# Optimization experiments

Hardware: AMD Instinct MI355X
Metric: run time of the kernel (lower is better)

Reference implementation:

```python
import jax, jax.numpy as jnp
import numpy as np

B, N, D = 4, 4096, 256
EPS = 1e-5


def setup_inputs() -> dict:
    key = jax.random.key(0)
    ks = jax.random.split(key, 6)
    x = jax.random.normal(ks[0], (B, N, D), dtype=jnp.float32)
    coord = jax.random.normal(ks[1], (B, N, D), dtype=jnp.float32)
    ln_g = jnp.ones((D,), dtype=jnp.float32)
    ln_b = jnp.zeros((D,), dtype=jnp.float32)
    s = 1.0 / np.sqrt(D)
    w_qkv = jax.random.normal(ks[2], (D, 3 * D), dtype=jnp.float32) * s
    w_out = jax.random.normal(ks[3], (D, D), dtype=jnp.float32) * s
    b_out = jnp.zeros((D,), dtype=jnp.float32)
    return {"x": x, "coord": coord, "ln_g": ln_g, "ln_b": ln_b,
            "w_qkv": w_qkv, "w_out": w_out, "b_out": b_out}


def reference(x, coord, ln_g, ln_b, w_qkv, w_out, b_out):
    d = x.shape[-1]
    scale = d ** (-0.5)
    # LayerNorm over last dim
    mu = jnp.mean(x, axis=-1, keepdims=True)
    var = jnp.var(x, axis=-1, keepdims=True)
    nx = (x - mu) * jax.lax.rsqrt(var + EPS) * ln_g + ln_b
    # QKV projection (no bias), chunk into q,k,v
    qkv = jnp.einsum('bnd,de->bne', nx, w_qkv)
    q, k, v = jnp.split(qkv, 3, axis=-1)
    # coord bias on q and k (module does NOT split into heads)
    q = q + coord
    k = k + coord
    dots = jnp.einsum('bnd,bmd->bnm', q, k) * scale
    attn = jax.nn.softmax(dots, axis=-1)
    out = jnp.einsum('bnm,bmd->bnd', attn, v)
    return jnp.einsum('bnd,de->bne', out, w_out) + b_out
```

## Files before the change

### kernel.cpp

```cpp
#include <hip/hip_runtime.h>
#include <hip/hip_fp16.h>
#include <math.h>

constexpr int B = 4, N = 4096, D = 256;
constexpr int BN = B * N;
constexpr float EPS = 1e-5f;
constexpr float QSC2 = 0.0625f * 1.44269504088896340736f;

constexpr int SPLIT = 4;
constexpr int KVB = 32;
constexpr int NTK = (N / SPLIT) / KVB;
constexpr float THR = 8.0f;

typedef __attribute__((ext_vector_type(8))) _Float16 f16x8;
typedef __attribute__((ext_vector_type(2))) __fp16 fp16x2;
typedef __attribute__((ext_vector_type(4))) float f32x4;
typedef __attribute__((ext_vector_type(16))) float f32x16;

__device__ inline f32x4 mfma_f16(f16x8 a, f16x8 b, f32x4 c) {
  return __builtin_amdgcn_mfma_f32_16x16x32_f16(a, b, c, 0, 0, 0);
}
__device__ inline f32x16 mfma32(f16x8 a, f16x8 b, f32x16 c) {
  return __builtin_amdgcn_mfma_f32_32x32x16_f16(a, b, c, 0, 0, 0);
}
__device__ inline ushort f2h(float x) {
  __half h = __float2half(x);
  return *(ushort*)&h;
}
__device__ inline float h2f(ushort u) {
  __half h;
  *(ushort*)&h = u;
  return __half2float(h);
}
__device__ inline unsigned pkh(float a, float b) {
  fp16x2 r = __builtin_amdgcn_cvt_pkrtz(a, b);
  return *(unsigned*)&r;
}
__device__ inline void gload16(const ushort* g, ushort* l) {
  __builtin_amdgcn_global_load_lds(
      (const __attribute__((address_space(1))) void*)g,
      (__attribute__((address_space(3))) void*)l, 16, 0, 0);
}

__global__ __launch_bounds__(256) void ln_kernel(
    const float* __restrict__ x, const float* __restrict__ g,
    const float* __restrict__ bta, ushort* __restrict__ nxh,
    ushort* __restrict__ nxl) {
  const int row = blockIdx.x;
  const int t = threadIdx.x;
  const float v = x[(size_t)row * D + t];
  float s = v, ss = v * v;
#pragma unroll
  for (int o = 32; o > 0; o >>= 1) {
    s += __shfl_down(s, o);
    ss += __shfl_down(ss, o);
  }
  __shared__ float red[8];
  if ((t & 63) == 0) {
    red[t >> 6] = s;
    red[(t >> 6) + 4] = ss;
  }
  __syncthreads();
  s = red[0] + red[1] + red[2] + red[3];
  ss = red[4] + red[5] + red[6] + red[7];
  const float mu = s * (1.0f / D);
  const float var = ss * (1.0f / D) - mu * mu;
  const float rsig = rsqrtf(var + EPS);
  const float nx = (v - mu) * rsig * g[t] + bta[t];
  const ushort h = f2h(nx);
  nxh[(size_t)row * D + t] = h;
  nxl[(size_t)row * D + t] = f2h(nx - h2f(h));
}

__global__ __launch_bounds__(256) void castw_kernel(
    const float* __restrict__ w_qkv, const float* __restrict__ w_out,
    ushort* __restrict__ wt, ushort* __restrict__ wot) {
  const int id = blockIdx.x * 256 + threadIdx.x;
  if (id < 768 * 256) {
    const int n = id >> 8, k = id & 255;
    wt[id] = f2h(w_qkv[(size_t)k * 768 + n]);
  } else {
    const int j = id - 768 * 256;
    const int n = j >> 8, k = j & 255;
    wot[j] = f2h(w_out[(size_t)k * 256 + n]);
  }
}

__global__ __launch_bounds__(256, 4) void qkv_kernel(
    const ushort* __restrict__ nxh, const ushort* __restrict__ nxl,
    const ushort* __restrict__ wt, const float* __restrict__ coord,
    ushort* __restrict__ qfp, ushort* __restrict__ kfp,
    ushort* __restrict__ vtp) {
  const int t = threadIdx.x;
  const int w = t >> 6, lane = t & 63;
  const int lrow = lane & 15, lhi = lane >> 4;
  const int m0 = blockIdx.x * 128 + w * 32;
  const int c0 = blockIdx.y * 64;
  f32x4 acc[2][4];
#pragma unroll
  for (int qs = 0; qs < 2; ++qs)
#pragma unroll
    for (int nt = 0; nt < 4; ++nt) acc[qs][nt] = f32x4{0.f, 0.f, 0.f, 0.f};

#pragma unroll
  for (int kc = 0; kc < D; kc += 32) {
    f16x8 ah[2], al[2], bw[4];
#pragma unroll
    for (int qs = 0; qs < 2; ++qs) {
      const size_t ao = (size_t)(m0 + qs * 16 + lrow) * D + kc + lhi * 8;
      ah[qs] = *(const f16x8*)(nxh + ao);
      al[qs] = *(const f16x8*)(nxl + ao);
    }
#pragma unroll
    for (int nt = 0; nt < 4; ++nt)
      bw[nt] = *(const f16x8*)(wt + (size_t)(c0 + nt * 16 + lrow) * D + kc +
                               lhi * 8);
#pragma unroll
    for (int qs = 0; qs < 2; ++qs)
#pragma unroll
      for (int nt = 0; nt < 4; ++nt) {
        acc[qs][nt] = mfma_f16(ah[qs], bw[nt], acc[qs][nt]);
        acc[qs][nt] = mfma_f16(al[qs], bw[nt], acc[qs][nt]);
      }
  }

  const int region = blockIdx.y >> 2;
  const int cbase = c0 & 255;
  if (region < 2) {
    const float sc = (region == 0) ? QSC2 : 1.0f;
    ushort* dp = (region == 0) ? qfp : kfp;
#pragma unroll
    for (int qs = 0; qs < 2; ++qs)
#pragma unroll
      for (int nt = 0; nt < 4; ++nt)
#pragma unroll
        for (int i = 0; i < 4; ++i) {
          const int row = m0 + qs * 16 + lhi * 4 + i;
          const int col = cbase + nt * 16 + lrow;
          const float val =
              (acc[qs][nt][i] + coord[(size_t)row * D + col]) * sc;
          dp[(size_t)row * D + col] = f2h(val);
        }
  } else {
#pragma unroll
    for (int qs = 0; qs < 2; ++qs)
#pragma unroll
      for (int nt = 0; nt < 4; ++nt)
#pragma unroll
        for (int i = 0; i < 4; ++i) {
          const int row = m0 + qs * 16 + lhi * 4 + i;
          const int col = cbase + nt * 16 + lrow;
          const int bb = row >> 12, n = row & (N - 1);
          vtp[((size_t)bb * D + col) * N + n] = f2h(acc[qs][nt][i]);
        }
  }
}

__global__ __launch_bounds__(512, 2) void attn_kernel(
    const ushort* __restrict__ qf, const ushort* __restrict__ kf,
    const ushort* __restrict__ vt, ushort* __restrict__ pob,
    float* __restrict__ mlb) {
  __shared__ ushort kbuf[3][8192];
  __shared__ ushort vbuf[3][8192];

  const int tid = threadIdx.x;
  const int lane = tid & 63;
  const int q = lane & 31, h = lane >> 5;
  const int w = tid >> 6;
  const int b = blockIdx.y, s = blockIdx.z;
  const int qw = blockIdx.x * 256 + w * 32;
  const int kbeg = s * (N / SPLIT);

  const ushort* qrow = qf + ((size_t)b * N + qw + q) * D;
  const ushort* kfb = kf + (size_t)b * N * D;
  const ushort* vtb = vt + (size_t)b * D * N;
  ushort* pog = pob + (size_t)s * BN * D;
  float* mlg = mlb + (size_t)s * BN * 2;

  f16x8 qfr[8];
#pragma unroll
  for (int c = 0; c < 8; ++c)
    qfr[c] = *(const f16x8*)(qrow + c * 16 + h * 8);

  f32x16 o[8];
#pragma unroll
  for (int dt = 0; dt < 8; ++dt)
#pragma unroll
    for (int r = 0; r < 16; ++r) o[dt][r] = 0.f;
  float m = -1e30f, lsum = 0.f;

  auto stage = [&](int bi, int k0) {
#pragma unroll
    for (int i = 0; i < 2; ++i) {
      const int g = i * 512 + tid;
      const int key = g >> 5, slot = g & 31;
      gload16(kfb + (size_t)(k0 + key) * D + ((slot ^ (key & 7)) * 8),
              &kbuf[bi][g * 8]);
    }
#pragma unroll
    for (int i = 0; i < 2; ++i) {
      const int g = i * 512 + tid;
      const int d = g >> 2, sg = g & 3;
      gload16(vtb + (size_t)d * N + k0 + ((sg ^ (d & 3)) * 8),
              &vbuf[bi][g * 8]);
    }
  };

  stage(0, kbeg);

  for (int t = 0; t < NTK; ++t) {
    const int cur = t % 3;
    f16x8 qs[8];
#pragma unroll
    for (int c = 0; c < 8; ++c)
      qs[c] = *(const f16x8*)(qrow + (8 + c) * 16 + h * 8);
    if (t + 1 < NTK) {
      stage((t + 1) % 3, kbeg + (t + 1) * KVB);
      asm volatile("s_waitcnt vmcnt(12)" ::: "memory");
    } else {
      asm volatile("s_waitcnt vmcnt(8)" ::: "memory");
    }
    __builtin_amdgcn_sched_barrier(0);
    __builtin_amdgcn_s_barrier();
    __builtin_amdgcn_sched_barrier(0);

    f32x16 pa, pb;
#pragma unroll
    for (int r = 0; r < 16; ++r) { pa[r] = 0.f; pb[r] = 0.f; }
    const int ksw = (q & 7);
    __builtin_amdgcn_s_setprio(1);
#pragma unroll
    for (int c = 0; c < 8; ++c) {
      const f16x8 ka = *(const f16x8*)&kbuf[cur][q * 256 +
                                                 (((c * 2 + h) ^ ksw) * 8)];
      const f16x8 kb_ = *(const f16x8*)&kbuf[cur][q * 256 +
                                                  ((((c + 8) * 2 + h) ^ ksw) * 8)];
      pa = mfma32(ka, qfr[c], pa);
      pb = mfma32(kb_, qs[c], pb);
    }
    __builtin_amdgcn_s_setprio(0);
    f32x16 p;
#pragma unroll
    for (int r = 0; r < 16; ++r) p[r] = pa[r] + pb[r];

    float tm[8];
#pragma unroll
    for (int j = 0; j < 8; ++j) tm[j] = fmaxf(p[2 * j], p[2 * j + 1]);
    float pmax = fmaxf(fmaxf(fmaxf(tm[0], tm[1]), fmaxf(tm[2], tm[3])),
                       fmaxf(fmaxf(tm[4], tm[5]), fmaxf(tm[6], tm[7])));
    const float pm = fmaxf(pmax, __shfl_xor(pmax, 32));
    const bool need = pm > m + THR;
    if (__any(need)) {
      const float mn = fmaxf(m, pm);
      const float f = exp2f(m - mn);
      m = mn;
      lsum *= f;
#pragma unroll
      for (int dt = 0; dt < 8; ++dt) o[dt] *= f;
    }
#pragma unroll
    for (int r = 0; r < 16; ++r) {
      p[r] = exp2f(p[r] - m);
      lsum += p[r];
    }

    f16x8 pf[2];
#pragma unroll
    for (int kk = 0; kk < 2; ++kk) {
      const int sub = kk * 8;
      unsigned x = pkh(p[sub + 0], p[sub + 1]);
      unsigned z = pkh(p[sub + 2], p[sub + 3]);
      unsigned y = pkh(p[sub + 4], p[sub + 5]);
      unsigned wv = pkh(p[sub + 6], p[sub + 7]);
      const unsigned xs = __shfl_xor(x, 32);
      const unsigned zs = __shfl_xor(z, 32);
      const unsigned ys = __shfl_xor(y, 32);
      const unsigned ws = __shfl_xor(wv, 32);
      union { f16x8 v; unsigned u[4]; } pu;
      pu.u[0] = h ? ys : x;
      pu.u[1] = h ? ws : z;
      pu.u[2] = h ? y : xs;
      pu.u[3] = h ? wv : zs;
      pf[kk] = pu.v;
    }

    __builtin_amdgcn_s_setprio(1);
#pragma unroll
    for (int dt = 0; dt < 8; ++dt) {
      const int d = dt * 32 + q;
      const int dsw = d & 3;
#pragma unroll
      for (int kk = 0; kk < 2; ++kk) {
        const f16x8 vf = *(const f16x8*)&vbuf[cur][d * 32 +
                                                   (((kk * 2 + h) ^ dsw) * 8)];
        o[dt] = mfma32(vf, pf[kk], o[dt]);
      }
    }
    __builtin_amdgcn_s_setprio(0);
  }

  const float lt = lsum + __shfl_xor(lsum, 32);
  const float inv = 1.0f / lt;
  ushort* orow = pog + ((size_t)b * N + qw + q) * D;
#pragma unroll
  for (int dt = 0; dt < 8; ++dt)
#pragma unroll
    for (int r4 = 0; r4 < 4; ++r4) {
      const unsigned u0 =
          pkh(o[dt][r4 * 4 + 0] * inv, o[dt][r4 * 4 + 1] * inv);
      const unsigned u1 =
          pkh(o[dt][r4 * 4 + 2] * inv, o[dt][r4 * 4 + 3] * inv);
      uint2 val;
      val.x = u0;
      val.y = u1;
      *(uint2*)(orow + dt * 32 + r4 * 8 + h * 4) = val;
    }
  if (h == 0) {
    const size_t r = (size_t)b * N + qw + q;
    mlg[r * 2] = m;
    mlg[r * 2 + 1] = lt;
  }
}

__global__ __launch_bounds__(256) void merge_kernel(
    const ushort* __restrict__ pob, const float* __restrict__ mlb,
    ushort* __restrict__ aoh, ushort* __restrict__ aol) {
  const int t = threadIdx.x;
  const int row = blockIdx.x * 8 + (t >> 5);
  const int d0 = (t & 31) * 8;
  float mv[SPLIT], lv[SPLIT];
  float mm = -1e30f;
#pragma unroll
  for (int s = 0; s < SPLIT; ++s) {
    mv[s] = mlb[(size_t)s * BN * 2 + row * 2];
    lv[s] = mlb[(size_t)s * BN * 2 + row * 2 + 1];
    mm = fmaxf(mm, mv[s]);
  }
  float wsum = 0.f, a[SPLIT];
#pragma unroll
  for (int s = 0; s < SPLIT; ++s) {
    a[s] = exp2f(mv[s] - mm) * lv[s];
    wsum += a[s];
  }
  const float invw = 1.0f / wsum;
  const size_t off = (size_t)row * D + d0;
  float r[8] = {};
#pragma unroll
  for (int s = 0; s < SPLIT; ++s) {
    const f16x8 p = *(const f16x8*)(pob + (size_t)s * BN * D + off);
    const float c = a[s] * invw;
#pragma unroll
    for (int j = 0; j < 8; ++j) r[j] += c * (float)p[j];
  }
  f16x8 rh, rl;
#pragma unroll
  for (int j = 0; j < 8; ++j) {
    rh[j] = (_Float16)r[j];
    rl[j] = (_Float16)(r[j] - (float)rh[j]);
  }
  *(f16x8*)(aoh + off) = rh;
  *(f16x8*)(aol + off) = rl;
}

__global__ __launch_bounds__(256, 4) void proj_kernel(
    const ushort* __restrict__ aoh, const ushort* __restrict__ aol,
    const ushort* __restrict__ wot, const float* __restrict__ bias,
    float* __restrict__ out) {
  const int t = threadIdx.x;
  const int w = t >> 6, lane = t & 63;
  const int lrow = lane & 15, lhi = lane >> 4;
  const int m0 = blockIdx.x * 128 + w * 32;
  const int c0 = blockIdx.y * 64;
  f32x4 acc[2][4];
#pragma unroll
  for (int qs = 0; qs < 2; ++qs)
#pragma unroll
    for (int nt = 0; nt < 4; ++nt) acc[qs][nt] = f32x4{0.f, 0.f, 0.f, 0.f};

#pragma unroll
  for (int kc = 0; kc < D; kc += 32) {
    f16x8 ah[2], al[2], bw[4];
#pragma unroll
    for (int qs = 0; qs < 2; ++qs) {
      const size_t ao = (size_t)(m0 + qs * 16 + lrow) * D + kc + lhi * 8;
      ah[qs] = *(const f16x8*)(aoh + ao);
      al[qs] = *(const f16x8*)(aol + ao);
    }
#pragma unroll
    for (int nt = 0; nt < 4; ++nt)
      bw[nt] = *(const f16x8*)(wot + (size_t)(c0 + nt * 16 + lrow) * D + kc +
                               lhi * 8);
#pragma unroll
    for (int qs = 0; qs < 2; ++qs)
#pragma unroll
      for (int nt = 0; nt < 4; ++nt) {
        acc[qs][nt] = mfma_f16(ah[qs], bw[nt], acc[qs][nt]);
        acc[qs][nt] = mfma_f16(al[qs], bw[nt], acc[qs][nt]);
      }
  }
#pragma unroll
  for (int qs = 0; qs < 2; ++qs)
#pragma unroll
    for (int nt = 0; nt < 4; ++nt)
#pragma unroll
      for (int i = 0; i < 4; ++i) {
        const int row = m0 + qs * 16 + lhi * 4 + i;
        const int col = c0 + nt * 16 + lrow;
        out[(size_t)row * D + col] = acc[qs][nt][i] + bias[col];
      }
}

extern "C" void kernel_launch(void* const* d_in, const int* in_sizes, int n_in,
                              void* d_out, int out_size, void* d_ws, size_t ws_size,
                              hipStream_t stream) {
  const float* x = (const float*)d_in[0];
  const float* coord = (const float*)d_in[1];
  const float* ln_g = (const float*)d_in[2];
  const float* ln_b = (const float*)d_in[3];
  const float* w_qkv = (const float*)d_in[4];
  const float* w_out = (const float*)d_in[5];
  const float* b_out = (const float*)d_in[6];
  float* out = (float*)d_out;

  const size_t P = (size_t)BN * D;

  ushort* qfp = (ushort*)d_ws;
  ushort* kfp = qfp + P;
  ushort* vtp = kfp + P;
  ushort* pob = vtp + P;
  float* mlb = (float*)(pob + (size_t)SPLIT * P);
  ushort* wt = (ushort*)(mlb + (size_t)SPLIT * BN * 2);
  ushort* wot = wt + 768 * 256;
  ushort* nxh = pob;
  ushort* nxl = pob + P;
  ushort* aoh = qfp;
  ushort* aol = kfp;

  hipLaunchKernelGGL(ln_kernel, dim3(BN), dim3(256), 0, stream,
                     x, ln_g, ln_b, nxh, nxl);
  hipLaunchKernelGGL(castw_kernel, dim3(1024), dim3(256), 0, stream,
                     w_qkv, w_out, wt, wot);
  hipLaunchKernelGGL(qkv_kernel, dim3(BN / 128, 12), dim3(256), 0, stream,
                     nxh, nxl, wt, coord, qfp, kfp, vtp);
  hipLaunchKernelGGL(attn_kernel, dim3(N / 256, B, SPLIT), dim3(512), 0,
                     stream, qfp, kfp, vtp, pob, mlb);
  hipLaunchKernelGGL(merge_kernel, dim3(BN / 8), dim3(256), 0, stream,
                     pob, mlb, aoh, aol);
  hipLaunchKernelGGL(proj_kernel, dim3(BN / 128, 4), dim3(256), 0, stream,
                     aoh, aol, wot, b_out, out);
}
```

Before: 210.5 us.

## Reswizzle V tile in LDS and unroll attention loop by triple-buffer period

Changes the shared-memory layout of the V tile so that two head-dim rows share a 64-element row with an 8-way XOR swizzle, replacing the old 4-way swizzle on 32-element rows. The goal is fewer LDS bank conflicts on the V reads feeding the MFMAs. The key loop is also unrolled by three via a macro, so buffer indices become compile-time constants and the per-iteration modulo and dynamic LDS addressing go away. The catch is larger code size and register pressure. The tail handling assumes NTK mod 3 equals 2, which holds for NTK=32.

```diff
diff --git a/kernel.cpp b/kernel.cpp
--- a/kernel.cpp
+++ b/kernel.cpp
@@ -200,104 +200,102 @@
 #pragma unroll
     for (int i = 0; i < 2; ++i) {
       const int g = i * 512 + tid;
-      const int d = g >> 2, sg = g & 3;
-      gload16(vtb + (size_t)d * N + k0 + ((sg ^ (d & 3)) * 8),
-              &vbuf[bi][g * 8]);
+      const int r = g >> 3, slot = g & 7;
+      const int u = slot ^ (r & 7);
+      const int d = r * 2 + (u >> 2);
+      gload16(vtb + (size_t)d * N + k0 + ((u & 3) * 8), &vbuf[bi][g * 8]);
     }
   };
 
   stage(0, kbeg);
 
-  for (int t = 0; t < NTK; ++t) {
-    const int cur = t % 3;
-    f16x8 qs[8];
-#pragma unroll
-    for (int c = 0; c < 8; ++c)
-      qs[c] = *(const f16x8*)(qrow + (8 + c) * 16 + h * 8);
-    if (t + 1 < NTK) {
-      stage((t + 1) % 3, kbeg + (t + 1) * KVB);
-      asm volatile("s_waitcnt vmcnt(12)" ::: "memory");
-    } else {
-      asm volatile("s_waitcnt vmcnt(8)" ::: "memory");
-    }
-    __builtin_amdgcn_sched_barrier(0);
-    __builtin_amdgcn_s_barrier();
-    __builtin_amdgcn_sched_barrier(0);
-
-    f32x16 pa, pb;
-#pragma unroll
-    for (int r = 0; r < 16; ++r) { pa[r] = 0.f; pb[r] = 0.f; }
-    const int ksw = (q & 7);
-    __builtin_amdgcn_s_setprio(1);
-#pragma unroll
-    for (int c = 0; c < 8; ++c) {
-      const f16x8 ka = *(const f16x8*)&kbuf[cur][q * 256 +
-                                                 (((c * 2 + h) ^ ksw) * 8)];
-      const f16x8 kb_ = *(const f16x8*)&kbuf[cur][q * 256 +
-                                                  ((((c + 8) * 2 + h) ^ ksw) * 8)];
-      pa = mfma32(ka, qfr[c], pa);
-      pb = mfma32(kb_, qs[c], pb);
-    }
-    __builtin_amdgcn_s_setprio(0);
-    f32x16 p;
-#pragma unroll
-    for (int r = 0; r < 16; ++r) p[r] = pa[r] + pb[r];
-
-    float tm[8];
-#pragma unroll
-    for (int j = 0; j < 8; ++j) tm[j] = fmaxf(p[2 * j], p[2 * j + 1]);
-    float pmax = fmaxf(fmaxf(fmaxf(tm[0], tm[1]), fmaxf(tm[2], tm[3])),
-                       fmaxf(fmaxf(tm[4], tm[5]), fmaxf(tm[6], tm[7])));
-    const float pm = fmaxf(pmax, __shfl_xor(pmax, 32));
-    const bool need = pm > m + THR;
-    if (__any(need)) {
-      const float mn = fmaxf(m, pm);
-      const float f = exp2f(m - mn);
-      m = mn;
-      lsum *= f;
-#pragma unroll
-      for (int dt = 0; dt < 8; ++dt) o[dt] *= f;
-    }
-#pragma unroll
-    for (int r = 0; r < 16; ++r) {
-      p[r] = exp2f(p[r] - m);
-      lsum += p[r];
-    }
-
-    f16x8 pf[2];
-#pragma unroll
-    for (int kk = 0; kk < 2; ++kk) {
-      const int sub = kk * 8;
-      unsigned x = pkh(p[sub + 0], p[sub + 1]);
-      unsigned z = pkh(p[sub + 2], p[sub + 3]);
-      unsigned y = pkh(p[sub + 4], p[sub + 5]);
-      unsigned wv = pkh(p[sub + 6], p[sub + 7]);
-      const unsigned xs = __shfl_xor(x, 32);
-      const unsigned zs = __shfl_xor(z, 32);
-      const unsigned ys = __shfl_xor(y, 32);
-      const unsigned ws = __shfl_xor(wv, 32);
-      union { f16x8 v; unsigned u[4]; } pu;
-      pu.u[0] = h ? ys : x;
-      pu.u[1] = h ? ws : z;
-      pu.u[2] = h ? y : xs;
-      pu.u[3] = h ? wv : zs;
-      pf[kk] = pu.v;
-    }
-
-    __builtin_amdgcn_s_setprio(1);
-#pragma unroll
-    for (int dt = 0; dt < 8; ++dt) {
-      const int d = dt * 32 + q;
-      const int dsw = d & 3;
-#pragma unroll
-      for (int kk = 0; kk < 2; ++kk) {
-        const f16x8 vf = *(const f16x8*)&vbuf[cur][d * 32 +
-                                                   (((kk * 2 + h) ^ dsw) * 8)];
-        o[dt] = mfma32(vf, pf[kk], o[dt]);
-      }
-    }
-    __builtin_amdgcn_s_setprio(0);
-  }
+#define ATTN_BODY(CUR, T, LASTB)                                             \
+  {                                                                          \
+    f16x8 qs[8];                                                             \
+    _Pragma("unroll") for (int c = 0; c < 8; ++c)                            \
+        qs[c] = *(const f16x8*)(qrow + (8 + c) * 16 + h * 8);                \
+    if (!(LASTB)) {                                                          \
+      stage(((CUR) + 1) % 3, kbeg + ((T) + 1) * KVB);                        \
+      asm volatile("s_waitcnt vmcnt(12)" ::: "memory");                      \
+    } else {                                                                 \
+      asm volatile("s_waitcnt vmcnt(8)" ::: "memory");                       \
+    }                                                                        \
+    __builtin_amdgcn_sched_barrier(0);                                       \
+    __builtin_amdgcn_s_barrier();                                            \
+    __builtin_amdgcn_sched_barrier(0);                                       \
+    f32x16 pa, pb;                                                           \
+    _Pragma("unroll") for (int r = 0; r < 16; ++r) { pa[r] = 0.f; pb[r] = 0.f; } \
+    const int ksw = (q & 7);                                                 \
+    __builtin_amdgcn_s_setprio(1);                                           \
+    _Pragma("unroll") for (int c = 0; c < 8; ++c) {                          \
+      const f16x8 ka =                                                       \
+          *(const f16x8*)&kbuf[CUR][q * 256 + (((c * 2 + h) ^ ksw) * 8)];    \
+      const f16x8 kb_ = *(const f16x8*)&kbuf[CUR][q * 256 +                  \
+                                                  ((((c + 8) * 2 + h) ^ ksw) * 8)]; \
+      pa = mfma32(ka, qfr[c], pa);                                           \
+      pb = mfma32(kb_, qs[c], pb);                                           \
+    }                                                                        \
+    __builtin_amdgcn_s_setprio(0);                                           \
+    f32x16 p;                                                                \
+    _Pragma("unroll") for (int r = 0; r < 16; ++r) p[r] = pa[r] + pb[r];     \
+    float tm[8];                                                             \
+    _Pragma("unroll") for (int j = 0; j < 8; ++j)                            \
+        tm[j] = fmaxf(p[2 * j], p[2 * j + 1]);                               \
+    float pmax = fmaxf(fmaxf(fmaxf(tm[0], tm[1]), fmaxf(tm[2], tm[3])),      \
+                       fmaxf(fmaxf(tm[4], tm[5]), fmaxf(tm[6], tm[7])));     \
+    const float pm = fmaxf(pmax, __shfl_xor(pmax, 32));                      \
+    const bool need = pm > m + THR;                                          \
+    if (__any(need)) {                                                       \
+      const float mn = fmaxf(m, pm);                                         \
+      const float f = exp2f(m - mn);                                         \
+      m = mn;                                                                \
+      lsum *= f;                                                             \
+      _Pragma("unroll") for (int dt = 0; dt < 8; ++dt) o[dt] *= f;           \
+    }                                                                        \
+    _Pragma("unroll") for (int r = 0; r < 16; ++r) {                         \
+      p[r] = exp2f(p[r] - m);                                                 \
+      lsum += p[r];                                                          \
+    }                                                                        \
+    f16x8 pf[2];                                                             \
+    _Pragma("unroll") for (int kk = 0; kk < 2; ++kk) {                       \
+      const int sub = kk * 8;                                                \
+      unsigned x = pkh(p[sub + 0], p[sub + 1]);                              \
+      unsigned z = pkh(p[sub + 2], p[sub + 3]);                              \
+      unsigned y = pkh(p[sub + 4], p[sub + 5]);                              \
+      unsigned wv = pkh(p[sub + 6], p[sub + 7]);                             \
+      const unsigned xs = __shfl_xor(x, 32);                                 \
+      const unsigned zs = __shfl_xor(z, 32);                                 \
+      const unsigned ys = __shfl_xor(y, 32);                                 \
+      const unsigned ws = __shfl_xor(wv, 32);                                \
+      union { f16x8 v; unsigned u[4]; } pu;                                  \
+      pu.u[0] = h ? ys : x;                                                  \
+      pu.u[1] = h ? ws : z;                                                  \
+      pu.u[2] = h ? y : xs;                                                  \
+      pu.u[3] = h ? wv : zs;                                                 \
+      pf[kk] = pu.v;                                                         \
+    }                                                                        \
+    __builtin_amdgcn_s_setprio(1);                                           \
+    _Pragma("unroll") for (int dt = 0; dt < 8; ++dt) {                       \
+      const int d = dt * 32 + q;                                             \
+      const int rr = d >> 1;                                                 \
+      _Pragma("unroll") for (int kk = 0; kk < 2; ++kk) {                     \
+        const int u = (d & 1) * 4 + kk * 2 + h;                              \
+        const f16x8 vf = *(const f16x8*)&vbuf[CUR][rr * 64 +                 \
+                                                   ((u ^ (rr & 7)) * 8)];    \
+        o[dt] = mfma32(vf, pf[kk], o[dt]);                                   \
+      }                                                                      \
+    }                                                                        \
+    __builtin_amdgcn_s_setprio(0);                                           \
+  }
+
+  for (int tb = 0; tb < NTK - 2; tb += 3) {
+    ATTN_BODY(0, tb + 0, false);
+    ATTN_BODY(1, tb + 1, false);
+    ATTN_BODY(2, tb + 2, false);
+  }
+  ATTN_BODY(0, NTK - 2, false);
+  ATTN_BODY(1, NTK - 1, true);
+#undef ATTN_BODY
 
   const float lt = lsum + __shfl_xor(lsum, 32);
   const float inv = 1.0f / lt;
```

Result: slower. 284.2 us (+35.0%).
